# Performance work log

Hardware: AMD Instinct MI355X
Metric: run time of the kernel (lower is better)

The kernel has to match this reference:

```python
import jax, jax.numpy as jnp
import numpy as np

N = 50000
E = 800000
EPS = 1e-5


def gcn_conv(x, W, b, src, dst, n):
    # PyG GCNConv: h = xW; add self-loops; symmetric norm D^-1/2 A_hat D^-1/2; out = agg + bias
    h = x @ W                                            # [N, out]
    deg = jax.ops.segment_sum(jnp.ones_like(src, dtype=h.dtype), dst, num_segments=n) + 1.0
    inv_sqrt = jax.lax.rsqrt(deg)                        # [N]
    coef = inv_sqrt[src] * inv_sqrt[dst]                 # [E]
    agg = jax.ops.segment_sum(h[src] * coef[:, None], dst, num_segments=n)
    agg = agg + h * (inv_sqrt * inv_sqrt)[:, None]       # self-loop term
    return agg + b


def batchnorm(h, gamma, beta):
    mean = jnp.mean(h, axis=0)
    var = jnp.var(h, axis=0)
    return gamma * (h - mean) * jax.lax.rsqrt(var + EPS) + beta


def setup_inputs() -> dict:
    key = jax.random.key(0)
    ks = jax.random.split(key, 8)
    x = jax.random.normal(ks[0], (N, 128), dtype=jnp.float32)
    edge_index = jax.random.randint(ks[1], (2, E), 0, N, dtype=jnp.int64)
    s = 1.0 / np.sqrt(128)
    W1 = jax.random.uniform(ks[2], (128, 128), jnp.float32, -s, s)
    W2 = jax.random.uniform(ks[3], (128, 128), jnp.float32, -s, s)
    W3 = jax.random.uniform(ks[4], (128, 64), jnp.float32, -s, s)
    b1 = jnp.zeros((128,), jnp.float32)
    b2 = jnp.zeros((128,), jnp.float32)
    b3 = jnp.zeros((64,), jnp.float32)
    g1 = jnp.ones((128,), jnp.float32)
    bt1 = jnp.zeros((128,), jnp.float32)
    g2 = jnp.ones((128,), jnp.float32)
    bt2 = jnp.zeros((128,), jnp.float32)
    return {"x": x, "edge_index": edge_index, "W1": W1, "b1": b1, "g1": g1, "bt1": bt1,
            "W2": W2, "b2": b2, "g2": g2, "bt2": bt2, "W3": W3, "b3": b3}


def reference(x, edge_index, W1, b1, g1, bt1, W2, b2, g2, bt2, W3, b3):
    src, dst = edge_index[0], edge_index[1]
    h = gcn_conv(x, W1, b1, src, dst, N)
    h = jax.nn.relu(batchnorm(h, g1, bt1))
    h = gcn_conv(h, W2, b2, src, dst, N)
    h = jax.nn.relu(batchnorm(h, g2, bt2))
    out = gcn_conv(h, W3, b3, src, dst, N)
    return out
```

## Files before the change

### kernel.cpp

```cpp
#include <hip/hip_runtime.h>

#define N_NODES 50000
#define N_EDGES 800000
static constexpr float EPS = 1e-5f;
static constexpr int SCAN_NB = (N_NODES + 255) / 256;
static constexpr int GEMM_NB = (N_NODES + 63) / 64;
static constexpr int FILL_NB = (N_EDGES + 1023) / 1024;

using bf16x8 = __attribute__((ext_vector_type(8))) short;
using f32x4  = __attribute__((ext_vector_type(4))) float;

static __device__ __forceinline__ unsigned short f2bf(float f) {
    unsigned int u = __float_as_uint(f);
    return (unsigned short)((u + 0x7FFFu + ((u >> 16) & 1u)) >> 16);
}
static __device__ __forceinline__ float blo(unsigned int w) { return __uint_as_float(w << 16); }
static __device__ __forceinline__ float bhi(unsigned int w) { return __uint_as_float(w & 0xffff0000u); }

__global__ __launch_bounds__(256) void k_prep_wconv(
    const int* __restrict__ ei, int* __restrict__ deg, int* __restrict__ rank,
    const float* __restrict__ W1, const float* __restrict__ W2,
    const float* __restrict__ W3,
    unsigned short* __restrict__ Wf1, unsigned short* __restrict__ Wf2,
    unsigned short* __restrict__ Wf3) {
    if (blockIdx.x < FILL_NB) {
        int e0 = (blockIdx.x * 256 + threadIdx.x) * 4;
        if (e0 >= N_EDGES) return;
        int4 d4 = *(const int4*)&ei[N_EDGES + e0];
        int4 r;
        r.x = atomicAdd(&deg[d4.x], 1);
        r.y = atomicAdd(&deg[d4.y], 1);
        r.z = atomicAdd(&deg[d4.z], 1);
        r.w = atomicAdd(&deg[d4.w], 1);
        *(int4*)&rank[e0] = r;
    } else {
        int gid = (blockIdx.x - FILL_NB) * 256 + threadIdx.x;
        const float* W; unsigned short* Wf; int NCOL, idx;
        if (gid < 16384)      { W = W1; Wf = Wf1; NCOL = 128; idx = gid; }
        else if (gid < 32768) { W = W2; Wf = Wf2; NCOL = 128; idx = gid - 16384; }
        else                  { W = W3; Wf = Wf3; NCOL = 64;  idx = gid - 32768; }
        int j  = idx & 7;
        int l  = (idx >> 3) & 63;
        int s  = (idx >> 9) & 3;
        int tn = idx >> 11;
        int n = tn * 16 + (l & 15);
        int k = s * 32 + (l >> 4) * 8 + j;
        Wf[idx] = f2bf(W[k * NCOL + n]);
    }
}

__global__ __launch_bounds__(256) void k_scan1(const int* __restrict__ deg,
                                               int* __restrict__ excl,
                                               int* __restrict__ partials) {
    const int t = threadIdx.x;
    const int i = blockIdx.x * 256 + t;
    int v = (i < N_NODES) ? deg[i] : 0;
    __shared__ int sh[256];
    sh[t] = v;
    __syncthreads();
    for (int off = 1; off < 256; off <<= 1) {
        int u = (t >= off) ? sh[t - off] : 0;
        __syncthreads();
        sh[t] += u;
        __syncthreads();
    }
    if (i < N_NODES) excl[i] = sh[t] - v;
    if (t == 255) partials[blockIdx.x] = sh[t];
}

__global__ __launch_bounds__(256) void k_scan23(const int* __restrict__ excl,
                                                const int* __restrict__ partials,
                                                const int* __restrict__ deg,
                                                int* __restrict__ rowptr,
                                                float* __restrict__ inv_sqrt) {
    const int t = threadIdx.x;
    int v = (t < SCAN_NB) ? partials[t] : 0;
    __shared__ int sh[256];
    __shared__ int base_s;
    sh[t] = v;
    __syncthreads();
    for (int off = 1; off < 256; off <<= 1) {
        int u = (t >= off) ? sh[t - off] : 0;
        __syncthreads();
        sh[t] += u;
        __syncthreads();
    }
    if (t == blockIdx.x) base_s = sh[t] - v;
    __syncthreads();
    const int base = base_s;
    const int i = blockIdx.x * 256 + t;
    if (i < N_NODES) {
        rowptr[i] = excl[i] + base;
        inv_sqrt[i] = rsqrtf((float)deg[i] + 1.0f);
    }
    if (i == 0) rowptr[N_NODES] = N_EDGES;
}

template <int NCOL, bool BN, bool ABF16>
static __device__ __forceinline__ void gemm_body(
    int row0, int t,
    const void* __restrict__ Ap, const unsigned short* __restrict__ Wf,
    const float* __restrict__ stats,
    const float* __restrict__ gamma, const float* __restrict__ beta,
    unsigned short* __restrict__ H,
    unsigned short* As, float* sc_s, float* sh_s) {
    if (BN) {
        if (t < 128) {
            float s  = stats[t];
            float sq = stats[128 + t];
            float mean = s * (1.0f / N_NODES);
            float var  = sq * (1.0f / N_NODES) - mean * mean;
            float sc = gamma[t] * rsqrtf(var + EPS);
            sc_s[t] = sc;
            sh_s[t] = beta[t] - mean * sc;
        }
        __syncthreads();
    }

#pragma unroll
    for (int i = 0; i < 4; i++) {
        int q = i * 256 + t;
        int row = q >> 4;
        int c8  = (q & 15) * 8;
        int grow = row0 + row;
        float v[8];
        if (grow < N_NODES) {
            if (ABF16) {
                uint4 p = *(const uint4*)((const unsigned short*)Ap + (size_t)grow * 128 + c8);
                v[0] = blo(p.x); v[1] = bhi(p.x); v[2] = blo(p.y); v[3] = bhi(p.y);
                v[4] = blo(p.z); v[5] = bhi(p.z); v[6] = blo(p.w); v[7] = bhi(p.w);
            } else {
                const float* Af = (const float*)Ap + (size_t)grow * 128 + c8;
                float4 f0 = *(const float4*)Af;
                float4 f1 = *(const float4*)(Af + 4);
                v[0] = f0.x; v[1] = f0.y; v[2] = f0.z; v[3] = f0.w;
                v[4] = f1.x; v[5] = f1.y; v[6] = f1.z; v[7] = f1.w;
            }
        } else {
#pragma unroll
            for (int j = 0; j < 8; j++) v[j] = 0.f;
        }
        if (BN) {
#pragma unroll
            for (int j = 0; j < 8; j++)
                v[j] = fmaxf(fmaf(v[j], sc_s[c8 + j], sh_s[c8 + j]), 0.f);
        }
        uint4 pk;
        pk.x = (unsigned)f2bf(v[0]) | ((unsigned)f2bf(v[1]) << 16);
        pk.y = (unsigned)f2bf(v[2]) | ((unsigned)f2bf(v[3]) << 16);
        pk.z = (unsigned)f2bf(v[4]) | ((unsigned)f2bf(v[5]) << 16);
        pk.w = (unsigned)f2bf(v[6]) | ((unsigned)f2bf(v[7]) << 16);
        *(uint4*)&As[row * 136 + c8] = pk;
    }
    __syncthreads();

    const int wv = t >> 6;
    const int l  = t & 63;
    const int m  = l & 15;
    const int kq = l >> 4;

    bf16x8 afrag[4];
    const unsigned short* arow = &As[(wv * 16 + m) * 136 + kq * 8];
#pragma unroll
    for (int s = 0; s < 4; s++)
        afrag[s] = *(const bf16x8*)(arow + s * 32);

    constexpr int NT = NCOL / 16;
#pragma unroll
    for (int tn = 0; tn < NT; tn++) {
        f32x4 acc = {0.f, 0.f, 0.f, 0.f};
#pragma unroll
        for (int s = 0; s < 4; s++) {
            bf16x8 b = *(const bf16x8*)&Wf[(size_t)((tn * 4 + s) * 64 + l) * 8];
            acc = __builtin_amdgcn_mfma_f32_16x16x32_bf16(afrag[s], b, acc, 0, 0, 0);
        }
        int col = tn * 16 + m;
#pragma unroll
        for (int r = 0; r < 4; r++) {
            int row = row0 + wv * 16 + kq * 4 + r;
            if (row < N_NODES) H[(size_t)row * NCOL + col] = f2bf(acc[r]);
        }
    }
}

template <int NCOL>
__global__ __launch_bounds__(256) void k_gemm_bn(
    const unsigned short* __restrict__ A, const unsigned short* __restrict__ Wf,
    const float* __restrict__ stats,
    const float* __restrict__ gamma, const float* __restrict__ beta,
    unsigned short* __restrict__ H) {
    __shared__ unsigned short As[64 * 136];
    __shared__ float sc_s[128], sh_s[128];
    gemm_body<NCOL, true, true>(blockIdx.x * 64, threadIdx.x, A, Wf, stats,
                                gamma, beta, H, As, sc_s, sh_s);
}

__global__ __launch_bounds__(256) void k_gemm1_fill(
    const float* __restrict__ x, const unsigned short* __restrict__ Wf1,
    unsigned short* __restrict__ h1,
    const int* __restrict__ ei, const int* __restrict__ rank,
    const int* __restrict__ rowptr, int* __restrict__ esrc) {
    __shared__ unsigned short As[64 * 136];
    __shared__ float sc_s[128], sh_s[128];
    if (blockIdx.x < GEMM_NB) {
        gemm_body<128, false, false>(blockIdx.x * 64, threadIdx.x, x, Wf1,
                                     nullptr, nullptr, nullptr, h1, As, sc_s, sh_s);
    } else {
        int e0 = ((blockIdx.x - GEMM_NB) * 256 + threadIdx.x) * 4;
        if (e0 < N_EDGES) {
            int4 s4 = *(const int4*)&ei[e0];
            int4 d4 = *(const int4*)&ei[N_EDGES + e0];
            int4 r4 = *(const int4*)&rank[e0];
            int p0 = rowptr[d4.x] + r4.x;
            int p1 = rowptr[d4.y] + r4.y;
            int p2 = rowptr[d4.z] + r4.z;
            int p3 = rowptr[d4.w] + r4.w;
            esrc[p0] = s4.x;
            esrc[p1] = s4.y;
            esrc[p2] = s4.z;
            esrc[p3] = s4.w;
        }
    }
}

template <int F, bool OUTBF>
__global__ __launch_bounds__(256) void k_agg(const int* __restrict__ rowptr,
                                             const int* __restrict__ esrc,
                                             const float* __restrict__ inv_sqrt,
                                             const unsigned short* __restrict__ H,
                                             const float* __restrict__ bias,
                                             void* __restrict__ OUT) {
    constexpr int LPN = F / 8;
    constexpr int NPB = 256 / LPN;
    const int t = threadIdx.x;
    const int node = blockIdx.x * NPB + t / LPN;
    const int lane = t % LPN;
    if (node >= N_NODES) return;

    const uint4* __restrict__ Hv = (const uint4*)H;
    const int beg = rowptr[node];
    const int end = rowptr[node + 1];
    const float rsn = inv_sqrt[node];

    float acc[8];
#pragma unroll
    for (int i = 0; i < 8; i++) acc[i] = 0.f;

#define ACC8(P, C)                                                     \
    acc[0] = fmaf(blo((P).x), (C), acc[0]);                            \
    acc[1] = fmaf(bhi((P).x), (C), acc[1]);                            \
    acc[2] = fmaf(blo((P).y), (C), acc[2]);                            \
    acc[3] = fmaf(bhi((P).y), (C), acc[3]);                            \
    acc[4] = fmaf(blo((P).z), (C), acc[4]);                            \
    acc[5] = fmaf(bhi((P).z), (C), acc[5]);                            \
    acc[6] = fmaf(blo((P).w), (C), acc[6]);                            \
    acc[7] = fmaf(bhi((P).w), (C), acc[7]);

    int j = beg;
    for (; j + 3 < end; j += 4) {
        int s0 = esrc[j], s1 = esrc[j + 1], s2 = esrc[j + 2], s3 = esrc[j + 3];
        uint4 p0 = Hv[(size_t)s0 * LPN + lane];
        uint4 p1 = Hv[(size_t)s1 * LPN + lane];
        uint4 p2 = Hv[(size_t)s2 * LPN + lane];
        uint4 p3 = Hv[(size_t)s3 * LPN + lane];
        float c0 = inv_sqrt[s0] * rsn, c1 = inv_sqrt[s1] * rsn;
        float c2 = inv_sqrt[s2] * rsn, c3 = inv_sqrt[s3] * rsn;
        ACC8(p0, c0) ACC8(p1, c1) ACC8(p2, c2) ACC8(p3, c3)
    }
    for (; j < end; j++) {
        int s0 = esrc[j];
        float c0 = inv_sqrt[s0] * rsn;
        uint4 p0 = Hv[(size_t)s0 * LPN + lane];
        ACC8(p0, c0)
    }
#undef ACC8

    uint4 ps = Hv[(size_t)node * LPN + lane];
    float idv = rsn * rsn;
    float4 b0 = ((const float4*)bias)[lane * 2];
    float4 b1 = ((const float4*)bias)[lane * 2 + 1];
    acc[0] = fmaf(blo(ps.x), idv, acc[0]) + b0.x;
    acc[1] = fmaf(bhi(ps.x), idv, acc[1]) + b0.y;
    acc[2] = fmaf(blo(ps.y), idv, acc[2]) + b0.z;
    acc[3] = fmaf(bhi(ps.y), idv, acc[3]) + b0.w;
    acc[4] = fmaf(blo(ps.z), idv, acc[4]) + b1.x;
    acc[5] = fmaf(bhi(ps.z), idv, acc[5]) + b1.y;
    acc[6] = fmaf(blo(ps.w), idv, acc[6]) + b1.z;
    acc[7] = fmaf(bhi(ps.w), idv, acc[7]) + b1.w;

    if (OUTBF) {
        uint4 pk;
        pk.x = (unsigned)f2bf(acc[0]) | ((unsigned)f2bf(acc[1]) << 16);
        pk.y = (unsigned)f2bf(acc[2]) | ((unsigned)f2bf(acc[3]) << 16);
        pk.z = (unsigned)f2bf(acc[4]) | ((unsigned)f2bf(acc[5]) << 16);
        pk.w = (unsigned)f2bf(acc[6]) | ((unsigned)f2bf(acc[7]) << 16);
        ((uint4*)OUT)[(size_t)node * LPN + lane] = pk;
    } else {
        float4* o = (float4*)OUT + ((size_t)node * LPN + lane) * 2;
        o[0] = make_float4(acc[0], acc[1], acc[2], acc[3]);
        o[1] = make_float4(acc[4], acc[5], acc[6], acc[7]);
    }
}

__global__ __launch_bounds__(256) void k_stats(const unsigned short* __restrict__ A,
                                               float* __restrict__ stats) {
    const int t  = threadIdx.x;
    const int c4 = t & 31;
    const int rr = t >> 5;
    float4 sum = make_float4(0.f, 0.f, 0.f, 0.f);
    float4 sq  = make_float4(0.f, 0.f, 0.f, 0.f);
    for (int row = blockIdx.x * 8 + rr; row < N_NODES; row += gridDim.x * 8) {
        uint2 p = *(const uint2*)&A[(size_t)row * 128 + c4 * 4];
        float vx = blo(p.x), vy = bhi(p.x), vz = blo(p.y), vw = bhi(p.y);
        sum.x += vx; sum.y += vy; sum.z += vz; sum.w += vw;
        sq.x += vx * vx; sq.y += vy * vy; sq.z += vz * vz; sq.w += vw * vw;
    }
    __shared__ float4 red[2][8][32];
    red[0][rr][c4] = sum;
    red[1][rr][c4] = sq;
    __syncthreads();
    if (t < 32) {
        float4 s = make_float4(0.f, 0.f, 0.f, 0.f);
        float4 q = make_float4(0.f, 0.f, 0.f, 0.f);
#pragma unroll
        for (int i = 0; i < 8; i++) {
            float4 a = red[0][i][t];
            float4 b = red[1][i][t];
            s.x += a.x; s.y += a.y; s.z += a.z; s.w += a.w;
            q.x += b.x; q.y += b.y; q.z += b.z; q.w += b.w;
        }
        int c = t * 4;
        atomicAdd(&stats[c + 0], s.x); atomicAdd(&stats[c + 1], s.y);
        atomicAdd(&stats[c + 2], s.z); atomicAdd(&stats[c + 3], s.w);
        atomicAdd(&stats[128 + c + 0], q.x); atomicAdd(&stats[128 + c + 1], q.y);
        atomicAdd(&stats[128 + c + 2], q.z); atomicAdd(&stats[128 + c + 3], q.w);
    }
}

extern "C" void kernel_launch(void* const* d_in, const int* in_sizes, int n_in,
                              void* d_out, int out_size, void* d_ws, size_t ws_size,
                              hipStream_t stream) {
    const float* x   = (const float*)d_in[0];
    const int*   ei  = (const int*)d_in[1];
    const float* W1  = (const float*)d_in[2];
    const float* b1  = (const float*)d_in[3];
    const float* g1  = (const float*)d_in[4];
    const float* bt1 = (const float*)d_in[5];
    const float* W2  = (const float*)d_in[6];
    const float* b2  = (const float*)d_in[7];
    const float* g2  = (const float*)d_in[8];
    const float* bt2 = (const float*)d_in[9];
    const float* W3  = (const float*)d_in[10];
    const float* b3  = (const float*)d_in[11];
    float* out = (float*)d_out;

    char* ws = (char*)d_ws;
    size_t off = 0;
    auto alloc = [&](size_t bytes) { char* p = ws + off; off += (bytes + 255) & ~(size_t)255; return p; };
    int*   deg      = (int*)  alloc((size_t)N_NODES * 4);
    float* stats1   = (float*)alloc(256 * 4);
    float* stats2   = (float*)alloc(256 * 4);
    const size_t zbytes = (size_t)((char*)(stats2 + 256) - (char*)deg);
    float* inv_sqrt = (float*)alloc((size_t)N_NODES * 4);
    int*   excl     = (int*)  alloc((size_t)N_NODES * 4);
    int*   partials = (int*)  alloc(256 * 4);
    int*   rowptr   = (int*)  alloc((size_t)(N_NODES + 1) * 4);
    int*   rank     = (int*)  alloc((size_t)N_EDGES * 4);
    int*   esrc     = (int*)  alloc((size_t)N_EDGES * 4);
    unsigned short* Wf1 = (unsigned short*)alloc((size_t)128 * 128 * 2);
    unsigned short* Wf2 = (unsigned short*)alloc((size_t)128 * 128 * 2);
    unsigned short* Wf3 = (unsigned short*)alloc((size_t)64 * 128 * 2);
    unsigned short* h1  = (unsigned short*)alloc((size_t)N_NODES * 128 * 2);
    unsigned short* h2  = (unsigned short*)alloc((size_t)N_NODES * 128 * 2);
    unsigned short* h3  = (unsigned short*)alloc((size_t)N_NODES * 64 * 2);
    unsigned short* agg1 = (unsigned short*)alloc((size_t)N_NODES * 128 * 2);
    unsigned short* agg2 = (unsigned short*)alloc((size_t)N_NODES * 128 * 2);

    hipMemsetAsync(deg, 0, zbytes, stream);

    k_prep_wconv<<<FILL_NB + 160, 256, 0, stream>>>(ei, deg, rank, W1, W2, W3,
                                                    Wf1, Wf2, Wf3);
    k_scan1<<<SCAN_NB, 256, 0, stream>>>(deg, excl, partials);
    k_scan23<<<SCAN_NB, 256, 0, stream>>>(excl, partials, deg, rowptr, inv_sqrt);

    k_gemm1_fill<<<GEMM_NB + FILL_NB, 256, 0, stream>>>(x, Wf1, h1, ei, rank, rowptr, esrc);

    k_agg<128, true><<<N_NODES / 16, 256, 0, stream>>>(rowptr, esrc, inv_sqrt, h1, b1, agg1);
    k_stats<<<256, 256, 0, stream>>>(agg1, stats1);

    k_gemm_bn<128><<<GEMM_NB, 256, 0, stream>>>(agg1, Wf2, stats1, g1, bt1, h2);
    k_agg<128, true><<<N_NODES / 16, 256, 0, stream>>>(rowptr, esrc, inv_sqrt, h2, b2, agg2);
    k_stats<<<256, 256, 0, stream>>>(agg2, stats2);

    k_gemm_bn<64><<<GEMM_NB, 256, 0, stream>>>(agg2, Wf3, stats2, g2, bt2, h3);
    k_agg<64, false><<<(N_NODES + 31) / 32, 256, 0, stream>>>(rowptr, esrc, inv_sqrt, h3, b3, out);
}
```

Baseline: 320.6 us.

## Regroup preprocessing launches, replace memset with kernel zeroing, unroll aggregation by eight

The memset is folded into the weight-conversion kernel as a grid-stride zeroing loop. Degree counting now runs alongside the first GEMM, inv_sqrt is computed in the first scan pass, and the CSR fill runs inside the second scan kernel using shared block offsets instead of a materialised rowptr. Together this drops one launch and one serial dependency from the preprocessing chain. The aggregation inner loop now handles eight neighbours at a time with vectorised int4 index loads to raise memory-level parallelism. The cost is more register pressure, and the int4 loads of esrc start at arbitrary row offsets, so they are not always 16-byte aligned.

```diff
diff --git a/kernel.cpp b/kernel.cpp
--- a/kernel.cpp
+++ b/kernel.cpp
@@ -17,83 +17,26 @@
 static __device__ __forceinline__ float blo(unsigned int w) { return __uint_as_float(w << 16); }
 static __device__ __forceinline__ float bhi(unsigned int w) { return __uint_as_float(w & 0xffff0000u); }
 
-__global__ __launch_bounds__(256) void k_prep_wconv(
-    const int* __restrict__ ei, int* __restrict__ deg, int* __restrict__ rank,
+__global__ __launch_bounds__(256) void k_wconv_zero(
     const float* __restrict__ W1, const float* __restrict__ W2,
     const float* __restrict__ W3,
     unsigned short* __restrict__ Wf1, unsigned short* __restrict__ Wf2,
-    unsigned short* __restrict__ Wf3) {
-    if (blockIdx.x < FILL_NB) {
-        int e0 = (blockIdx.x * 256 + threadIdx.x) * 4;
-        if (e0 >= N_EDGES) return;
-        int4 d4 = *(const int4*)&ei[N_EDGES + e0];
-        int4 r;
-        r.x = atomicAdd(&deg[d4.x], 1);
-        r.y = atomicAdd(&deg[d4.y], 1);
-        r.z = atomicAdd(&deg[d4.z], 1);
-        r.w = atomicAdd(&deg[d4.w], 1);
-        *(int4*)&rank[e0] = r;
-    } else {
-        int gid = (blockIdx.x - FILL_NB) * 256 + threadIdx.x;
-        const float* W; unsigned short* Wf; int NCOL, idx;
-        if (gid < 16384)      { W = W1; Wf = Wf1; NCOL = 128; idx = gid; }
-        else if (gid < 32768) { W = W2; Wf = Wf2; NCOL = 128; idx = gid - 16384; }
-        else                  { W = W3; Wf = Wf3; NCOL = 64;  idx = gid - 32768; }
-        int j  = idx & 7;
-        int l  = (idx >> 3) & 63;
-        int s  = (idx >> 9) & 3;
-        int tn = idx >> 11;
-        int n = tn * 16 + (l & 15);
-        int k = s * 32 + (l >> 4) * 8 + j;
-        Wf[idx] = f2bf(W[k * NCOL + n]);
-    }
-}
-
-__global__ __launch_bounds__(256) void k_scan1(const int* __restrict__ deg,
-                                               int* __restrict__ excl,
-                                               int* __restrict__ partials) {
-    const int t = threadIdx.x;
-    const int i = blockIdx.x * 256 + t;
-    int v = (i < N_NODES) ? deg[i] : 0;
-    __shared__ int sh[256];
-    sh[t] = v;
-    __syncthreads();
-    for (int off = 1; off < 256; off <<= 1) {
-        int u = (t >= off) ? sh[t - off] : 0;
-        __syncthreads();
-        sh[t] += u;
-        __syncthreads();
-    }
-    if (i < N_NODES) excl[i] = sh[t] - v;
-    if (t == 255) partials[blockIdx.x] = sh[t];
-}
-
-__global__ __launch_bounds__(256) void k_scan23(const int* __restrict__ excl,
-                                                const int* __restrict__ partials,
-                                                const int* __restrict__ deg,
-                                                int* __restrict__ rowptr,
-                                                float* __restrict__ inv_sqrt) {
-    const int t = threadIdx.x;
-    int v = (t < SCAN_NB) ? partials[t] : 0;
-    __shared__ int sh[256];
-    __shared__ int base_s;
-    sh[t] = v;
-    __syncthreads();
-    for (int off = 1; off < 256; off <<= 1) {
-        int u = (t >= off) ? sh[t - off] : 0;
-        __syncthreads();
-        sh[t] += u;
-        __syncthreads();
-    }
-    if (t == blockIdx.x) base_s = sh[t] - v;
-    __syncthreads();
-    const int base = base_s;
-    const int i = blockIdx.x * 256 + t;
-    if (i < N_NODES) {
-        rowptr[i] = excl[i] + base;
-        inv_sqrt[i] = rsqrtf((float)deg[i] + 1.0f);
-    }
-    if (i == 0) rowptr[N_NODES] = N_EDGES;
+    unsigned short* __restrict__ Wf3,
+    int4* __restrict__ zbase, int zero16) {
+    int gid = blockIdx.x * 256 + threadIdx.x;
+    for (int i = gid; i < zero16; i += 160 * 256)
+        zbase[i] = make_int4(0, 0, 0, 0);
+    const float* W; unsigned short* Wf; int NCOL, idx;
+    if (gid < 16384)      { W = W1; Wf = Wf1; NCOL = 128; idx = gid; }
+    else if (gid < 32768) { W = W2; Wf = Wf2; NCOL = 128; idx = gid - 16384; }
+    else                  { W = W3; Wf = Wf3; NCOL = 64;  idx = gid - 32768; }
+    int j  = idx & 7;
+    int l  = (idx >> 3) & 63;
+    int s  = (idx >> 9) & 3;
+    int tn = idx >> 11;
+    int n = tn * 16 + (l & 15);
+    int k = s * 32 + (l >> 4) * 8 + j;
+    Wf[idx] = f2bf(W[k * NCOL + n]);
 }
 
 template <int NCOL, bool BN, bool ABF16>
@@ -195,26 +138,84 @@
                                 gamma, beta, H, As, sc_s, sh_s);
 }
 
-__global__ __launch_bounds__(256) void k_gemm1_fill(
+__global__ __launch_bounds__(256) void k_prep_gemm1(
+    const int* __restrict__ ei, int* __restrict__ deg, int* __restrict__ rank,
     const float* __restrict__ x, const unsigned short* __restrict__ Wf1,
-    unsigned short* __restrict__ h1,
-    const int* __restrict__ ei, const int* __restrict__ rank,
-    const int* __restrict__ rowptr, int* __restrict__ esrc) {
+    unsigned short* __restrict__ h1) {
     __shared__ unsigned short As[64 * 136];
     __shared__ float sc_s[128], sh_s[128];
-    if (blockIdx.x < GEMM_NB) {
-        gemm_body<128, false, false>(blockIdx.x * 64, threadIdx.x, x, Wf1,
-                                     nullptr, nullptr, nullptr, h1, As, sc_s, sh_s);
+    if (blockIdx.x < FILL_NB) {
+        int e0 = (blockIdx.x * 256 + threadIdx.x) * 4;
+        if (e0 >= N_EDGES) return;
+        int4 d4 = *(const int4*)&ei[N_EDGES + e0];
+        int4 r;
+        r.x = atomicAdd(&deg[d4.x], 1);
+        r.y = atomicAdd(&deg[d4.y], 1);
+        r.z = atomicAdd(&deg[d4.z], 1);
+        r.w = atomicAdd(&deg[d4.w], 1);
+        *(int4*)&rank[e0] = r;
     } else {
-        int e0 = ((blockIdx.x - GEMM_NB) * 256 + threadIdx.x) * 4;
+        gemm_body<128, false, false>((blockIdx.x - FILL_NB) * 64, threadIdx.x,
+                                     x, Wf1, nullptr, nullptr, nullptr, h1,
+                                     As, sc_s, sh_s);
+    }
+}
+
+__global__ __launch_bounds__(256) void k_scan1(const int* __restrict__ deg,
+                                               float* __restrict__ inv_sqrt,
+                                               int* __restrict__ excl,
+                                               int* __restrict__ partials) {
+    const int t = threadIdx.x;
+    const int i = blockIdx.x * 256 + t;
+    int v = (i < N_NODES) ? deg[i] : 0;
+    if (i < N_NODES) inv_sqrt[i] = rsqrtf((float)v + 1.0f);
+    __shared__ int sh[256];
+    sh[t] = v;
+    __syncthreads();
+    for (int off = 1; off < 256; off <<= 1) {
+        int u = (t >= off) ? sh[t - off] : 0;
+        __syncthreads();
+        sh[t] += u;
+        __syncthreads();
+    }
+    if (i < N_NODES) excl[i] = sh[t] - v;
+    if (t == 255) partials[blockIdx.x] = sh[t];
+}
+
+__global__ __launch_bounds__(256) void k_scan23_fill(
+    const int* __restrict__ excl, const int* __restrict__ partials,
+    int* __restrict__ rowptr,
+    const int* __restrict__ ei, const int* __restrict__ rank,
+    int* __restrict__ esrc) {
+    const int t = threadIdx.x;
+    __shared__ int sh[256];
+    __shared__ int ps[256];
+    int v = (t < SCAN_NB) ? partials[t] : 0;
+    sh[t] = v;
+    __syncthreads();
+    for (int off = 1; off < 256; off <<= 1) {
+        int u = (t >= off) ? sh[t - off] : 0;
+        __syncthreads();
+        sh[t] += u;
+        __syncthreads();
+    }
+    ps[t] = sh[t] - v;
+    __syncthreads();
+
+    if (blockIdx.x < SCAN_NB) {
+        const int i = blockIdx.x * 256 + t;
+        if (i < N_NODES) rowptr[i] = excl[i] + ps[blockIdx.x];
+        if (i == 0) rowptr[N_NODES] = N_EDGES;
+    } else {
+        int e0 = ((blockIdx.x - SCAN_NB) * 256 + t) * 4;
         if (e0 < N_EDGES) {
             int4 s4 = *(const int4*)&ei[e0];
             int4 d4 = *(const int4*)&ei[N_EDGES + e0];
             int4 r4 = *(const int4*)&rank[e0];
-            int p0 = rowptr[d4.x] + r4.x;
-            int p1 = rowptr[d4.y] + r4.y;
-            int p2 = rowptr[d4.z] + r4.z;
-            int p3 = rowptr[d4.w] + r4.w;
+            int p0 = excl[d4.x] + ps[d4.x >> 8] + r4.x;
+            int p1 = excl[d4.y] + ps[d4.y >> 8] + r4.y;
+            int p2 = excl[d4.z] + ps[d4.z >> 8] + r4.z;
+            int p3 = excl[d4.w] + ps[d4.w >> 8] + r4.w;
             esrc[p0] = s4.x;
             esrc[p1] = s4.y;
             esrc[p2] = s4.z;
@@ -257,15 +258,34 @@
     acc[7] = fmaf(bhi((P).w), (C), acc[7]);
 
     int j = beg;
-    for (; j + 3 < end; j += 4) {
-        int s0 = esrc[j], s1 = esrc[j + 1], s2 = esrc[j + 2], s3 = esrc[j + 3];
-        uint4 p0 = Hv[(size_t)s0 * LPN + lane];
-        uint4 p1 = Hv[(size_t)s1 * LPN + lane];
-        uint4 p2 = Hv[(size_t)s2 * LPN + lane];
-        uint4 p3 = Hv[(size_t)s3 * LPN + lane];
-        float c0 = inv_sqrt[s0] * rsn, c1 = inv_sqrt[s1] * rsn;
-        float c2 = inv_sqrt[s2] * rsn, c3 = inv_sqrt[s3] * rsn;
+    for (; j + 7 < end; j += 8) {
+        int4 sa = *(const int4*)&esrc[j];
+        int4 sb = *(const int4*)&esrc[j + 4];
+        uint4 p0 = Hv[(size_t)sa.x * LPN + lane];
+        uint4 p1 = Hv[(size_t)sa.y * LPN + lane];
+        uint4 p2 = Hv[(size_t)sa.z * LPN + lane];
+        uint4 p3 = Hv[(size_t)sa.w * LPN + lane];
+        uint4 p4 = Hv[(size_t)sb.x * LPN + lane];
+        uint4 p5 = Hv[(size_t)sb.y * LPN + lane];
+        uint4 p6 = Hv[(size_t)sb.z * LPN + lane];
+        uint4 p7 = Hv[(size_t)sb.w * LPN + lane];
+        float c0 = inv_sqrt[sa.x] * rsn, c1 = inv_sqrt[sa.y] * rsn;
+        float c2 = inv_sqrt[sa.z] * rsn, c3 = inv_sqrt[sa.w] * rsn;
+        float c4 = inv_sqrt[sb.x] * rsn, c5 = inv_sqrt[sb.y] * rsn;
+        float c6 = inv_sqrt[sb.z] * rsn, c7 = inv_sqrt[sb.w] * rsn;
         ACC8(p0, c0) ACC8(p1, c1) ACC8(p2, c2) ACC8(p3, c3)
+        ACC8(p4, c4) ACC8(p5, c5) ACC8(p6, c6) ACC8(p7, c7)
+    }
+    if (j + 3 < end) {
+        int4 sa = *(const int4*)&esrc[j];
+        uint4 p0 = Hv[(size_t)sa.x * LPN + lane];
+        uint4 p1 = Hv[(size_t)sa.y * LPN + lane];
+        uint4 p2 = Hv[(size_t)sa.z * LPN + lane];
+        uint4 p3 = Hv[(size_t)sa.w * LPN + lane];
+        float c0 = inv_sqrt[sa.x] * rsn, c1 = inv_sqrt[sa.y] * rsn;
+        float c2 = inv_sqrt[sa.z] * rsn, c3 = inv_sqrt[sa.w] * rsn;
+        ACC8(p0, c0) ACC8(p1, c1) ACC8(p2, c2) ACC8(p3, c3)
+        j += 4;
     }
     for (; j < end; j++) {
         int s0 = esrc[j];
@@ -361,6 +381,7 @@
     float* stats1   = (float*)alloc(256 * 4);
     float* stats2   = (float*)alloc(256 * 4);
     const size_t zbytes = (size_t)((char*)(stats2 + 256) - (char*)deg);
+    const int zero16 = (int)(zbytes / 16);
     float* inv_sqrt = (float*)alloc((size_t)N_NODES * 4);
     int*   excl     = (int*)  alloc((size_t)N_NODES * 4);
     int*   partials = (int*)  alloc(256 * 4);
@@ -376,22 +397,17 @@
     unsigned short* agg1 = (unsigned short*)alloc((size_t)N_NODES * 128 * 2);
     unsigned short* agg2 = (unsigned short*)alloc((size_t)N_NODES * 128 * 2);
 
-    hipMemsetAsync(deg, 0, zbytes, stream);
-
-    k_prep_wconv<<<FILL_NB + 160, 256, 0, stream>>>(ei, deg, rank, W1, W2, W3,
-                                                    Wf1, Wf2, Wf3);
-    k_scan1<<<SCAN_NB, 256, 0, stream>>>(deg, excl, partials);
-    k_scan23<<<SCAN_NB, 256, 0, stream>>>(excl, partials, deg, rowptr, inv_sqrt);
-
-    k_gemm1_fill<<<GEMM_NB + FILL_NB, 256, 0, stream>>>(x, Wf1, h1, ei, rank, rowptr, esrc);
-
+    k_wconv_zero<<<160, 256, 0, stream>>>(W1, W2, W3, Wf1, Wf2, Wf3,
+                                          (int4*)deg, zero16);
+    k_prep_gemm1<<<FILL_NB + GEMM_NB, 256, 0, stream>>>(ei, deg, rank, x, Wf1, h1);
+    k_scan1<<<SCAN_NB, 256, 0, stream>>>(deg, inv_sqrt, excl, partials);
+    k_scan23_fill<<<SCAN_NB + FILL_NB, 256, 0, stream>>>(excl, partials, rowptr,
+                                                         ei, rank, esrc);
     k_agg<128, true><<<N_NODES / 16, 256, 0, stream>>>(rowptr, esrc, inv_sqrt, h1, b1, agg1);
     k_stats<<<256, 256, 0, stream>>>(agg1, stats1);
-
     k_gemm_bn<128><<<GEMM_NB, 256, 0, stream>>>(agg1, Wf2, stats1, g1, bt1, h2);
     k_agg<128, true><<<N_NODES / 16, 256, 0, stream>>>(rowptr, esrc, inv_sqrt, h2, b2, agg2);
     k_stats<<<256, 256, 0, stream>>>(agg2, stats2);
-
     k_gemm_bn<64><<<GEMM_NB, 256, 0, stream>>>(agg2, Wf3, stats2, g2, bt2, h3);
     k_agg<64, false><<<(N_NODES + 31) / 32, 256, 0, stream>>>(rowptr, esrc, inv_sqrt, h3, b3, out);
 }
```

Result: no change. 321.1 us (+0.2%).
